# Performance work log

Hardware: AMD Instinct MI355X
Metric: run time of the kernel (lower is better)

Reference implementation:

```python
import jax, jax.numpy as jnp
import numpy as np

B, N, F_IN, F_OUT, H = 8, 1024, 256, 256, 4
HD = F_OUT // H  # head_dim = 64
NEG_SLOPE = 0.2


def setup_inputs() -> dict:
    key = jax.random.key(0)
    k1, k2, k3 = jax.random.split(key, 3)
    x = jax.random.normal(k1, (B, N, F_IN), dtype=jnp.float32)
    adj = jnp.ones((B, N, N), dtype=jnp.int32)
    # Linear weight, stored as [in, out] so h = x @ W
    W = jax.random.normal(k2, (F_IN, F_OUT), dtype=jnp.float32) / np.sqrt(F_IN)
    # attention vector a: [H, 2*head_dim], xavier-ish init
    a = jax.random.normal(k3, (H, 2 * HD), dtype=jnp.float32) * np.sqrt(2.0 / (H + 2 * HD))
    return {"x": x, "adj": adj, "W": W, "a": a}


def reference(x, adj, W, a):
    Bq, Nq, _ = x.shape
    h = (x @ W).reshape(Bq, Nq, H, HD).transpose(0, 2, 1, 3)  # [B,H,N,HD]
    a1, a2 = a[:, :HD], a[:, HD:]  # decompose concat: e_nm = h_n.a1 + h_m.a2
    s1 = jnp.einsum('bhnd,hd->bhn', h, a1)
    s2 = jnp.einsum('bhmd,hd->bhm', h, a2)
    e = jax.nn.leaky_relu(s1[:, :, :, None] + s2[:, :, None, :], NEG_SLOPE)  # [B,H,N,N]
    e = jnp.where(adj[:, None, :, :] == 0, -jnp.inf, e)
    attention = jax.nn.softmax(e, axis=-1)
    out = jnp.einsum('bhnm,bhmd->bhnd', attention, h)
    return out.transpose(0, 2, 1, 3).reshape(Bq, Nq, H * HD)
```

## Files before the change

### kernel.cpp

```cpp
#include <hip/hip_runtime.h>
#include <math.h>

#define H 4
#define HD 64
#define NN 1024
#define BB 8
#define FIN 256
#define FOUT 256

typedef _Float16 f16x8 __attribute__((ext_vector_type(8)));
typedef _Float16 f16x4 __attribute__((ext_vector_type(4)));
typedef _Float16 f16x2 __attribute__((ext_vector_type(2)));
typedef float f32x4 __attribute__((ext_vector_type(4)));

__global__ __launch_bounds__(256) void prep(const int* __restrict__ adj,
                                            unsigned* __restrict__ adjP,
                                            const float* __restrict__ W,
                                            _Float16* __restrict__ WT) {
  __shared__ float tile[64][68];
  const int tid = threadIdx.x;
  if (blockIdx.x < 1024) {
    size_t widx = (size_t)blockIdx.x * 256 + tid;
    const int4* p = (const int4*)adj + widx * 8;
    int4 v[8];
#pragma unroll
    for (int i = 0; i < 8; ++i) v[i] = p[i];
    unsigned bits = 0;
#pragma unroll
    for (int i = 0; i < 8; ++i) {
      bits |= (v[i].x != 0 ? 1u : 0u) << (4 * i);
      bits |= (v[i].y != 0 ? 2u : 0u) << (4 * i);
      bits |= (v[i].z != 0 ? 4u : 0u) << (4 * i);
      bits |= (v[i].w != 0 ? 8u : 0u) << (4 * i);
    }
    adjP[widx] = bits;
  } else {
    const int bx = blockIdx.x - 1024;
    const int k0 = (bx & 3) * 64, f0 = (bx >> 2) * 64;
    const int r = tid >> 4, c4 = (tid & 15) * 4;
#pragma unroll
    for (int p = 0; p < 4; ++p) {
      float4 v = *(const float4*)&W[(size_t)(k0 + p * 16 + r) * FOUT + f0 + c4];
      *(float4*)&tile[p * 16 + r][c4] = v;
    }
    __syncthreads();
    const int f = tid >> 2, kg = (tid & 3) * 16;
#pragma unroll
    for (int i = 0; i < 4; ++i) {
      f16x4 o;
#pragma unroll
      for (int j = 0; j < 4; ++j) o[j] = (_Float16)tile[kg + i * 4 + j][f];
      *(f16x4*)&WT[(size_t)(f0 + f) * FIN + k0 + kg + i * 4] = o;
    }
  }
}

__global__ __launch_bounds__(256) void gemm_xw(const float* __restrict__ x,
                                               const _Float16* __restrict__ WT,
                                               const float* __restrict__ a,
                                               _Float16* __restrict__ hT,
                                               float* __restrict__ s1_ws,
                                               float* __restrict__ s2_ws,
                                               float* __restrict__ u_ws,
                                               float* __restrict__ v_ws) {
  __shared__ _Float16 wl[64][264];
  const int tid = threadIdx.x;
  const int lane = tid & 63, w = tid >> 6;
  const int c = lane & 15, q = lane >> 4;
  const int bn0 = blockIdx.x * 64;
  const int head = blockIdx.y;
  const int b = bn0 >> 10, nb = bn0 & 1023;
  const int bh = b * H + head;

  {
    const int row = tid >> 2, kseg = (tid & 3) * 64;
    const _Float16* wp = WT + (size_t)(head * 64 + row) * FIN + kseg;
#pragma unroll
    for (int i = 0; i < 8; ++i) {
      f16x8 t = *(const f16x8*)(wp + i * 8);
      *(f16x8*)&wl[row][kseg + i * 8] = t;
    }
  }
  __syncthreads();

  f32x4 acc[4];
#pragma unroll
  for (int t = 0; t < 4; ++t) acc[t] = (f32x4){0.f, 0.f, 0.f, 0.f};
  const float* xp = x + (size_t)(bn0 + w * 16 + c) * FIN + q * 8;
#pragma unroll
  for (int ks = 0; ks < 8; ++ks) {
    float4 xa = *(const float4*)(xp + ks * 32);
    float4 xb = *(const float4*)(xp + ks * 32 + 4);
    f16x8 af;
    af[0] = (_Float16)xa.x; af[1] = (_Float16)xa.y;
    af[2] = (_Float16)xa.z; af[3] = (_Float16)xa.w;
    af[4] = (_Float16)xb.x; af[5] = (_Float16)xb.y;
    af[6] = (_Float16)xb.z; af[7] = (_Float16)xb.w;
#pragma unroll
    for (int t = 0; t < 4; ++t) {
      f16x8 bf = *(const f16x8*)&wl[t * 16 + c][ks * 32 + q * 8];
      acc[t] = __builtin_amdgcn_mfma_f32_16x16x32_f16(af, bf, acc[t], 0, 0, 0);
    }
  }

  float a1v[4], a2v[4];
#pragma unroll
  for (int t = 0; t < 4; ++t) {
    a1v[t] = a[head * 2 * HD + t * 16 + c];
    a2v[t] = a[head * 2 * HD + HD + t * 16 + c];
  }
  float s1p[4] = {0.f, 0.f, 0.f, 0.f};
  float s2p[4] = {0.f, 0.f, 0.f, 0.f};
#pragma unroll
  for (int t = 0; t < 4; ++t) {
    f16x4 hv;
#pragma unroll
    for (int rr = 0; rr < 4; ++rr) {
      hv[rr] = (_Float16)acc[t][rr];
      s1p[rr] += acc[t][rr] * a1v[t];
      s2p[rr] += acc[t][rr] * a2v[t];
    }
    *(f16x4*)&hT[((size_t)(bh * 64 + t * 16 + c)) * NN + nb + w * 16 + q * 4] = hv;
  }
#pragma unroll
  for (int rr = 0; rr < 4; ++rr) {
    float s1 = s1p[rr], s2 = s2p[rr];
#pragma unroll
    for (int off = 8; off; off >>= 1) {
      s1 += __shfl_xor(s1, off);
      s2 += __shfl_xor(s2, off);
    }
    if (c == 0) {
      int n = nb + w * 16 + q * 4 + rr;
      size_t idx = (size_t)bh * NN + n;
      s1_ws[idx] = s1;
      s2_ws[idx] = s2;
      u_ws[idx] = __expf(s2);
      v_ws[idx] = __expf(0.2f * s2);
    }
  }
}

__global__ __launch_bounds__(256) void attn(const _Float16* __restrict__ hT,
                                            const float* __restrict__ s1_ws,
                                            const float* __restrict__ s2_ws,
                                            const float* __restrict__ u_ws,
                                            const float* __restrict__ v_ws,
                                            const unsigned* __restrict__ adjP,
                                            float* __restrict__ out) {
  __shared__ float s2r[NN], uu[NN], vv[NN];
  __shared__ unsigned adjW[64][32];
  const int tid = threadIdx.x, lane = tid & 63, wv = tid >> 6;
  const int c = lane & 15, q = lane >> 4;
  const int ntile = blockIdx.x, bh = blockIdx.y;
  const int b = bh >> 2, head = bh & 3;
  const int n0 = ntile * 64;
  const int myrow = wv * 16 + c;

  {
    size_t base = (size_t)bh * NN + tid * 4;
    *(float4*)&s2r[tid * 4] = *(const float4*)&s2_ws[base];
    *(float4*)&uu[tid * 4] = *(const float4*)&u_ws[base];
    *(float4*)&vv[tid * 4] = *(const float4*)&v_ws[base];
    const int row = tid >> 2, wo = (tid & 3) * 8;
    const uint4* ap = (const uint4*)(adjP + ((size_t)(b * NN + n0 + row)) * 32 + wo);
    uint4 m0 = ap[0], m1 = ap[1];
    *(uint4*)&adjW[row][wo] = m0;
    *(uint4*)&adjW[row][wo + 4] = m1;
  }
  __syncthreads();

  const float s1 = s1_ws[(size_t)bh * NN + n0 + myrow];

  float mx = -INFINITY;
#pragma unroll 8
  for (int kc = 0; kc < 32; ++kc) {
    unsigned byte = (adjW[myrow][kc] >> (q * 8)) & 0xffu;
    float4 sa = *(const float4*)&s2r[kc * 32 + q * 8];
    float4 sb = *(const float4*)&s2r[kc * 32 + q * 8 + 4];
    mx = fmaxf(mx, (byte & 1u) ? sa.x : -INFINITY);
    mx = fmaxf(mx, (byte & 2u) ? sa.y : -INFINITY);
    mx = fmaxf(mx, (byte & 4u) ? sa.z : -INFINITY);
    mx = fmaxf(mx, (byte & 8u) ? sa.w : -INFINITY);
    mx = fmaxf(mx, (byte & 16u) ? sb.x : -INFINITY);
    mx = fmaxf(mx, (byte & 32u) ? sb.y : -INFINITY);
    mx = fmaxf(mx, (byte & 64u) ? sb.z : -INFINITY);
    mx = fmaxf(mx, (byte & 128u) ? sb.w : -INFINITY);
  }
  mx = fmaxf(mx, __shfl_xor(mx, 16));
  mx = fmaxf(mx, __shfl_xor(mx, 32));
  const float t0 = s1 + mx;
  const float M = fmaxf(t0, 0.2f * t0);
  const float Ar = __expf(s1 - M), Br = __expf(0.2f * s1 - M), ns1 = -s1;

  f32x4 acc[4];
#pragma unroll
  for (int t = 0; t < 4; ++t) acc[t] = (f32x4){0.f, 0.f, 0.f, 0.f};
  float psum = 0.f;
  const _Float16* bp0 = hT + ((size_t)bh * 64 + c) * NN + q * 8;

  f16x8 nbf[4];
#pragma unroll
  for (int t = 0; t < 4; ++t) nbf[t] = *(const f16x8*)(bp0 + (size_t)t * 16 * NN);

#pragma unroll 4
  for (int kc = 0; kc < 32; ++kc) {
    f16x8 bf[4];
#pragma unroll
    for (int t = 0; t < 4; ++t) bf[t] = nbf[t];
    unsigned byte = (adjW[myrow][kc] >> (q * 8)) & 0xffu;
    float4 sa = *(const float4*)&s2r[kc * 32 + q * 8];
    float4 sb = *(const float4*)&s2r[kc * 32 + q * 8 + 4];
    float4 ua = *(const float4*)&uu[kc * 32 + q * 8];
    float4 ub = *(const float4*)&uu[kc * 32 + q * 8 + 4];
    float4 va = *(const float4*)&vv[kc * 32 + q * 8];
    float4 vb = *(const float4*)&vv[kc * 32 + q * 8 + 4];
    float p0 = (sa.x >= ns1) ? Ar * ua.x : Br * va.x;
    float p1 = (sa.y >= ns1) ? Ar * ua.y : Br * va.y;
    float p2 = (sa.z >= ns1) ? Ar * ua.z : Br * va.z;
    float p3 = (sa.w >= ns1) ? Ar * ua.w : Br * va.w;
    float p4 = (sb.x >= ns1) ? Ar * ub.x : Br * vb.x;
    float p5 = (sb.y >= ns1) ? Ar * ub.y : Br * vb.y;
    float p6 = (sb.z >= ns1) ? Ar * ub.z : Br * vb.z;
    float p7 = (sb.w >= ns1) ? Ar * ub.w : Br * vb.w;
    p0 = (byte & 1u) ? p0 : 0.f;
    p1 = (byte & 2u) ? p1 : 0.f;
    p2 = (byte & 4u) ? p2 : 0.f;
    p3 = (byte & 8u) ? p3 : 0.f;
    p4 = (byte & 16u) ? p4 : 0.f;
    p5 = (byte & 32u) ? p5 : 0.f;
    p6 = (byte & 64u) ? p6 : 0.f;
    p7 = (byte & 128u) ? p7 : 0.f;
    psum += ((p0 + p1) + (p2 + p3)) + ((p4 + p5) + (p6 + p7));
    union { f16x8 v8; f16x2 v2[4]; } au;
    au.v2[0] = __builtin_bit_cast(f16x2, __builtin_amdgcn_cvt_pkrtz(p0, p1));
    au.v2[1] = __builtin_bit_cast(f16x2, __builtin_amdgcn_cvt_pkrtz(p2, p3));
    au.v2[2] = __builtin_bit_cast(f16x2, __builtin_amdgcn_cvt_pkrtz(p4, p5));
    au.v2[3] = __builtin_bit_cast(f16x2, __builtin_amdgcn_cvt_pkrtz(p6, p7));
    if (kc < 31) {
#pragma unroll
      for (int t = 0; t < 4; ++t)
        nbf[t] = *(const f16x8*)(bp0 + (size_t)t * 16 * NN + (kc + 1) * 32);
    }
#pragma unroll
    for (int t = 0; t < 4; ++t)
      acc[t] = __builtin_amdgcn_mfma_f32_16x16x32_f16(au.v8, bf[t], acc[t], 0, 0, 0);
  }

  psum += __shfl_xor(psum, 16);
  psum += __shfl_xor(psum, 32);
  float il[4];
#pragma unroll
  for (int rr = 0; rr < 4; ++rr) il[rr] = 1.0f / __shfl(psum, q * 4 + rr);
#pragma unroll
  for (int t = 0; t < 4; ++t) {
#pragma unroll
    for (int rr = 0; rr < 4; ++rr) {
      out[((size_t)(b * NN + n0 + wv * 16 + q * 4 + rr)) * FOUT + head * 64 + t * 16 + c] =
          acc[t][rr] * il[rr];
    }
  }
}

extern "C" void kernel_launch(void* const* d_in, const int* in_sizes, int n_in,
                              void* d_out, int out_size, void* d_ws, size_t ws_size,
                              hipStream_t stream) {
  const float* x = (const float*)d_in[0];
  const int* adj = (const int*)d_in[1];
  const float* W = (const float*)d_in[2];
  const float* a = (const float*)d_in[3];
  float* out = (float*)d_out;

  char* ws = (char*)d_ws;
  _Float16* hT = (_Float16*)ws;
  _Float16* WT = (_Float16*)(ws + (size_t)4 * 1024 * 1024);
  float* s1_ws = (float*)(ws + (size_t)4 * 1024 * 1024 + 128 * 1024);
  float* s2_ws = s1_ws + (size_t)BB * H * NN;
  float* u_ws = s2_ws + (size_t)BB * H * NN;
  float* v_ws = u_ws + (size_t)BB * H * NN;
  unsigned* adjP = (unsigned*)(v_ws + (size_t)BB * H * NN);

  prep<<<1040, 256, 0, stream>>>(adj, adjP, W, WT);
  gemm_xw<<<dim3(128, 4), 256, 0, stream>>>(x, WT, a, hT, s1_ws, s2_ws, u_ws, v_ws);
  attn<<<dim3(16, 32), 256, 0, stream>>>(hT, s1_ws, s2_ws, u_ws, v_ws, adjP, out);
}
```

Measured before the change: 131.6 us.

## Use global s2 max bound and packed fp16 max trick in attention

Replaces the per-row masked max pass with a per-(batch,head) global max of s2, computed via an order-preserving atomicMax in the projection kernel. Because leaky_relu(s1+s2) is the max of two linear terms, each probability becomes max(A*u, B*v), and the kernel evaluates this in packed fp16 from fp16 u/v tables. Row sums are produced by an extra MFMA against a ones vector instead of scalar adds. A block-level dense flag lets fully-connected tiles skip the mask entirely. Work is remapped so each wave owns 16 output features across all 64 rows. The cost is fp16 precision in the probabilities, with possible underflow when a row's max sits far below the global bound, and double the MFMA count.

```diff
diff --git a/kernel.cpp b/kernel.cpp
--- a/kernel.cpp
+++ b/kernel.cpp
@@ -13,10 +13,20 @@
 typedef _Float16 f16x2 __attribute__((ext_vector_type(2)));
 typedef float f32x4 __attribute__((ext_vector_type(4)));
 
+__device__ __forceinline__ unsigned fkey(float f) {
+  unsigned u = __float_as_uint(f);
+  return (u & 0x80000000u) ? ~u : (u | 0x80000000u);
+}
+__device__ __forceinline__ float fdecode(unsigned k) {
+  unsigned u = (k & 0x80000000u) ? (k & 0x7fffffffu) : ~k;
+  return __uint_as_float(u);
+}
+
 __global__ __launch_bounds__(256) void prep(const int* __restrict__ adj,
                                             unsigned* __restrict__ adjP,
                                             const float* __restrict__ W,
-                                            _Float16* __restrict__ WT) {
+                                            _Float16* __restrict__ WT,
+                                            unsigned* __restrict__ S2maxU) {
   __shared__ float tile[64][68];
   const int tid = threadIdx.x;
   if (blockIdx.x < 1024) {
@@ -35,6 +45,7 @@
     }
     adjP[widx] = bits;
   } else {
+    if (blockIdx.x == 1024 && tid < 32) S2maxU[tid] = 0u;
     const int bx = blockIdx.x - 1024;
     const int k0 = (bx & 3) * 64, f0 = (bx >> 2) * 64;
     const int r = tid >> 4, c4 = (tid & 15) * 4;
@@ -61,8 +72,7 @@
                                                _Float16* __restrict__ hT,
                                                float* __restrict__ s1_ws,
                                                float* __restrict__ s2_ws,
-                                               float* __restrict__ u_ws,
-                                               float* __restrict__ v_ws) {
+                                               unsigned* __restrict__ S2maxU) {
   __shared__ _Float16 wl[64][264];
   const int tid = threadIdx.x;
   const int lane = tid & 63, w = tid >> 6;
@@ -122,6 +132,7 @@
     }
     *(f16x4*)&hT[((size_t)(bh * 64 + t * 16 + c)) * NN + nb + w * 16 + q * 4] = hv;
   }
+  float ms2 = -INFINITY;
 #pragma unroll
   for (int rr = 0; rr < 4; ++rr) {
     float s1 = s1p[rr], s2 = s2p[rr];
@@ -130,134 +141,139 @@
       s1 += __shfl_xor(s1, off);
       s2 += __shfl_xor(s2, off);
     }
+    ms2 = fmaxf(ms2, s2);
     if (c == 0) {
       int n = nb + w * 16 + q * 4 + rr;
       size_t idx = (size_t)bh * NN + n;
       s1_ws[idx] = s1;
       s2_ws[idx] = s2;
-      u_ws[idx] = __expf(s2);
-      v_ws[idx] = __expf(0.2f * s2);
-    }
-  }
+    }
+  }
+  ms2 = fmaxf(ms2, __shfl_xor(ms2, 16));
+  ms2 = fmaxf(ms2, __shfl_xor(ms2, 32));
+  if (lane == 0) atomicMax(&S2maxU[bh], fkey(ms2));
 }
 
 __global__ __launch_bounds__(256) void attn(const _Float16* __restrict__ hT,
                                             const float* __restrict__ s1_ws,
                                             const float* __restrict__ s2_ws,
-                                            const float* __restrict__ u_ws,
-                                            const float* __restrict__ v_ws,
+                                            const unsigned* __restrict__ S2maxU,
                                             const unsigned* __restrict__ adjP,
                                             float* __restrict__ out) {
-  __shared__ float s2r[NN], uu[NN], vv[NN];
-  __shared__ unsigned adjW[64][32];
+  __shared__ _Float16 u16[NN], v16[NN];
+  __shared__ unsigned adjW[64][36];
+  __shared__ int denseFlag;
   const int tid = threadIdx.x, lane = tid & 63, wv = tid >> 6;
   const int c = lane & 15, q = lane >> 4;
   const int ntile = blockIdx.x, bh = blockIdx.y;
   const int b = bh >> 2, head = bh & 3;
   const int n0 = ntile * 64;
-  const int myrow = wv * 16 + c;
-
+
+  if (tid == 0) denseFlag = 1;
+  __syncthreads();
+
+  const float S2 = fdecode(S2maxU[bh]);
   {
-    size_t base = (size_t)bh * NN + tid * 4;
-    *(float4*)&s2r[tid * 4] = *(const float4*)&s2_ws[base];
-    *(float4*)&uu[tid * 4] = *(const float4*)&u_ws[base];
-    *(float4*)&vv[tid * 4] = *(const float4*)&v_ws[base];
+    float4 s2a = *(const float4*)&s2_ws[(size_t)bh * NN + tid * 4];
+    f16x4 ua, va;
+    ua[0] = (_Float16)__expf(s2a.x - S2); va[0] = (_Float16)__expf(0.2f * (s2a.x - S2));
+    ua[1] = (_Float16)__expf(s2a.y - S2); va[1] = (_Float16)__expf(0.2f * (s2a.y - S2));
+    ua[2] = (_Float16)__expf(s2a.z - S2); va[2] = (_Float16)__expf(0.2f * (s2a.z - S2));
+    ua[3] = (_Float16)__expf(s2a.w - S2); va[3] = (_Float16)__expf(0.2f * (s2a.w - S2));
+    *(f16x4*)&u16[tid * 4] = ua;
+    *(f16x4*)&v16[tid * 4] = va;
     const int row = tid >> 2, wo = (tid & 3) * 8;
     const uint4* ap = (const uint4*)(adjP + ((size_t)(b * NN + n0 + row)) * 32 + wo);
     uint4 m0 = ap[0], m1 = ap[1];
     *(uint4*)&adjW[row][wo] = m0;
     *(uint4*)&adjW[row][wo + 4] = m1;
+    unsigned andall = m0.x & m0.y & m0.z & m0.w & m1.x & m1.y & m1.z & m1.w;
+    if (andall != 0xffffffffu) atomicAnd(&denseFlag, 0);
   }
   __syncthreads();
-
-  const float s1 = s1_ws[(size_t)bh * NN + n0 + myrow];
-
-  float mx = -INFINITY;
-#pragma unroll 8
-  for (int kc = 0; kc < 32; ++kc) {
-    unsigned byte = (adjW[myrow][kc] >> (q * 8)) & 0xffu;
-    float4 sa = *(const float4*)&s2r[kc * 32 + q * 8];
-    float4 sb = *(const float4*)&s2r[kc * 32 + q * 8 + 4];
-    mx = fmaxf(mx, (byte & 1u) ? sa.x : -INFINITY);
-    mx = fmaxf(mx, (byte & 2u) ? sa.y : -INFINITY);
-    mx = fmaxf(mx, (byte & 4u) ? sa.z : -INFINITY);
-    mx = fmaxf(mx, (byte & 8u) ? sa.w : -INFINITY);
-    mx = fmaxf(mx, (byte & 16u) ? sb.x : -INFINITY);
-    mx = fmaxf(mx, (byte & 32u) ? sb.y : -INFINITY);
-    mx = fmaxf(mx, (byte & 64u) ? sb.z : -INFINITY);
-    mx = fmaxf(mx, (byte & 128u) ? sb.w : -INFINITY);
-  }
-  mx = fmaxf(mx, __shfl_xor(mx, 16));
-  mx = fmaxf(mx, __shfl_xor(mx, 32));
-  const float t0 = s1 + mx;
-  const float M = fmaxf(t0, 0.2f * t0);
-  const float Ar = __expf(s1 - M), Br = __expf(0.2f * s1 - M), ns1 = -s1;
-
-  f32x4 acc[4];
-#pragma unroll
-  for (int t = 0; t < 4; ++t) acc[t] = (f32x4){0.f, 0.f, 0.f, 0.f};
-  float psum = 0.f;
-  const _Float16* bp0 = hT + ((size_t)bh * 64 + c) * NN + q * 8;
-
-  f16x8 nbf[4];
-#pragma unroll
-  for (int t = 0; t < 4; ++t) nbf[t] = *(const f16x8*)(bp0 + (size_t)t * 16 * NN);
-
-#pragma unroll 4
-  for (int kc = 0; kc < 32; ++kc) {
-    f16x8 bf[4];
-#pragma unroll
-    for (int t = 0; t < 4; ++t) bf[t] = nbf[t];
-    unsigned byte = (adjW[myrow][kc] >> (q * 8)) & 0xffu;
-    float4 sa = *(const float4*)&s2r[kc * 32 + q * 8];
-    float4 sb = *(const float4*)&s2r[kc * 32 + q * 8 + 4];
-    float4 ua = *(const float4*)&uu[kc * 32 + q * 8];
-    float4 ub = *(const float4*)&uu[kc * 32 + q * 8 + 4];
-    float4 va = *(const float4*)&vv[kc * 32 + q * 8];
-    float4 vb = *(const float4*)&vv[kc * 32 + q * 8 + 4];
-    float p0 = (sa.x >= ns1) ? Ar * ua.x : Br * va.x;
-    float p1 = (sa.y >= ns1) ? Ar * ua.y : Br * va.y;
-    float p2 = (sa.z >= ns1) ? Ar * ua.z : Br * va.z;
-    float p3 = (sa.w >= ns1) ? Ar * ua.w : Br * va.w;
-    float p4 = (sb.x >= ns1) ? Ar * ub.x : Br * vb.x;
-    float p5 = (sb.y >= ns1) ? Ar * ub.y : Br * vb.y;
-    float p6 = (sb.z >= ns1) ? Ar * ub.z : Br * vb.z;
-    float p7 = (sb.w >= ns1) ? Ar * ub.w : Br * vb.w;
-    p0 = (byte & 1u) ? p0 : 0.f;
-    p1 = (byte & 2u) ? p1 : 0.f;
-    p2 = (byte & 4u) ? p2 : 0.f;
-    p3 = (byte & 8u) ? p3 : 0.f;
-    p4 = (byte & 16u) ? p4 : 0.f;
-    p5 = (byte & 32u) ? p5 : 0.f;
-    p6 = (byte & 64u) ? p6 : 0.f;
-    p7 = (byte & 128u) ? p7 : 0.f;
-    psum += ((p0 + p1) + (p2 + p3)) + ((p4 + p5) + (p6 + p7));
-    union { f16x8 v8; f16x2 v2[4]; } au;
-    au.v2[0] = __builtin_bit_cast(f16x2, __builtin_amdgcn_cvt_pkrtz(p0, p1));
-    au.v2[1] = __builtin_bit_cast(f16x2, __builtin_amdgcn_cvt_pkrtz(p2, p3));
-    au.v2[2] = __builtin_bit_cast(f16x2, __builtin_amdgcn_cvt_pkrtz(p4, p5));
-    au.v2[3] = __builtin_bit_cast(f16x2, __builtin_amdgcn_cvt_pkrtz(p6, p7));
-    if (kc < 31) {
-#pragma unroll
-      for (int t = 0; t < 4; ++t)
-        nbf[t] = *(const f16x8*)(bp0 + (size_t)t * 16 * NN + (kc + 1) * 32);
-    }
-#pragma unroll
-    for (int t = 0; t < 4; ++t)
-      acc[t] = __builtin_amdgcn_mfma_f32_16x16x32_f16(au.v8, bf[t], acc[t], 0, 0, 0);
-  }
-
-  psum += __shfl_xor(psum, 16);
-  psum += __shfl_xor(psum, 32);
-  float il[4];
-#pragma unroll
-  for (int rr = 0; rr < 4; ++rr) il[rr] = 1.0f / __shfl(psum, q * 4 + rr);
-#pragma unroll
-  for (int t = 0; t < 4; ++t) {
+  const int dense = denseFlag;
+
+  f16x2 ar2[4], br2[4];
+#pragma unroll
+  for (int g = 0; g < 4; ++g) {
+    float s1 = s1_ws[(size_t)bh * NN + n0 + g * 16 + c];
+    float t = s1 + S2;
+    float M = fmaxf(t, 0.2f * t);
+    _Float16 A = (_Float16)__expf(t - M);
+    _Float16 Bv = (_Float16)__expf(0.2f * t - M);
+    ar2[g][0] = A; ar2[g][1] = A;
+    br2[g][0] = Bv; br2[g][1] = Bv;
+  }
+
+  f32x4 acc[4], accL[4];
+#pragma unroll
+  for (int g = 0; g < 4; ++g) {
+    acc[g] = (f32x4){0.f, 0.f, 0.f, 0.f};
+    accL[g] = (f32x4){0.f, 0.f, 0.f, 0.f};
+  }
+  f16x8 bones;
+  {
+    _Float16 o = (c == 0) ? (_Float16)1.0f : (_Float16)0.0f;
+#pragma unroll
+    for (int j = 0; j < 8; ++j) bones[j] = o;
+  }
+
+  const _Float16* bp = hT + ((size_t)bh * 64 + wv * 16 + c) * NN + q * 8;
+  f16x8 nbf = *(const f16x8*)bp;
+
+  for (int kc4 = 0; kc4 < 8; ++kc4) {
+    unsigned mrow[4][4];
+    if (!dense) {
+#pragma unroll
+      for (int g = 0; g < 4; ++g) {
+        uint4 t = *(const uint4*)&adjW[g * 16 + c][kc4 * 4];
+        mrow[g][0] = t.x; mrow[g][1] = t.y; mrow[g][2] = t.z; mrow[g][3] = t.w;
+      }
+    }
+#pragma unroll
+    for (int kk = 0; kk < 4; ++kk) {
+      const int kc = kc4 * 4 + kk;
+      f16x8 bf = nbf;
+      if (kc < 31) nbf = *(const f16x8*)(bp + (kc + 1) * 32);
+      f16x8 u8 = *(const f16x8*)&u16[kc * 32 + q * 8];
+      f16x8 v8 = *(const f16x8*)&v16[kc * 32 + q * 8];
+      f16x2 up[4], vp[4];
+#pragma unroll
+      for (int j = 0; j < 4; ++j) {
+        up[j][0] = u8[2 * j]; up[j][1] = u8[2 * j + 1];
+        vp[j][0] = v8[2 * j]; vp[j][1] = v8[2 * j + 1];
+      }
+#pragma unroll
+      for (int g = 0; g < 4; ++g) {
+        f16x2 pp[4];
+#pragma unroll
+        for (int j = 0; j < 4; ++j)
+          pp[j] = __builtin_elementwise_max(ar2[g] * up[j], br2[g] * vp[j]);
+        if (!dense) {
+          unsigned byte = (mrow[g][kk] >> (q * 8)) & 0xffu;
+#pragma unroll
+          for (int j = 0; j < 4; ++j) {
+            unsigned pm = __builtin_bit_cast(unsigned, pp[j]);
+            unsigned msk = (((byte >> (2 * j)) & 1u) ? 0x0000ffffu : 0u) |
+                           (((byte >> (2 * j + 1)) & 1u) ? 0xffff0000u : 0u);
+            pp[j] = __builtin_bit_cast(f16x2, pm & msk);
+          }
+        }
+        union { f16x8 v8_; f16x2 v2_[4]; } au;
+        au.v2_[0] = pp[0]; au.v2_[1] = pp[1]; au.v2_[2] = pp[2]; au.v2_[3] = pp[3];
+        acc[g] = __builtin_amdgcn_mfma_f32_16x16x32_f16(au.v8_, bf, acc[g], 0, 0, 0);
+        accL[g] = __builtin_amdgcn_mfma_f32_16x16x32_f16(au.v8_, bones, accL[g], 0, 0, 0);
+      }
+    }
+  }
+
+#pragma unroll
+  for (int g = 0; g < 4; ++g) {
 #pragma unroll
     for (int rr = 0; rr < 4; ++rr) {
-      out[((size_t)(b * NN + n0 + wv * 16 + q * 4 + rr)) * FOUT + head * 64 + t * 16 + c] =
-          acc[t][rr] * il[rr];
+      float Lrow = __shfl(accL[g][rr], q * 16);
+      out[((size_t)(b * NN + n0 + g * 16 + q * 4 + rr)) * FOUT + head * 64 + wv * 16 + c] =
+          acc[g][rr] / Lrow;
     }
   }
 }
@@ -276,11 +292,10 @@
   _Float16* WT = (_Float16*)(ws + (size_t)4 * 1024 * 1024);
   float* s1_ws = (float*)(ws + (size_t)4 * 1024 * 1024 + 128 * 1024);
   float* s2_ws = s1_ws + (size_t)BB * H * NN;
-  float* u_ws = s2_ws + (size_t)BB * H * NN;
-  float* v_ws = u_ws + (size_t)BB * H * NN;
-  unsigned* adjP = (unsigned*)(v_ws + (size_t)BB * H * NN);
-
-  prep<<<1040, 256, 0, stream>>>(adj, adjP, W, WT);
-  gemm_xw<<<dim3(128, 4), 256, 0, stream>>>(x, WT, a, hT, s1_ws, s2_ws, u_ws, v_ws);
-  attn<<<dim3(16, 32), 256, 0, stream>>>(hT, s1_ws, s2_ws, u_ws, v_ws, adjP, out);
-}
+  unsigned* S2maxU = (unsigned*)(s2_ws + (size_t)BB * H * NN);
+  unsigned* adjP = S2maxU + 64;
+
+  prep<<<1040, 256, 0, stream>>>(adj, adjP, W, WT, S2maxU);
+  gemm_xw<<<dim3(128, 4), 256, 0, stream>>>(x, WT, a, hT, s1_ws, s2_ws, S2maxU);
+  attn<<<dim3(16, 32), 256, 0, stream>>>(hT, s1_ws, s2_ws, S2maxU, adjP, out);
+}
```

New measurement: 120.3 us. 8.6% less time.
